# Performance work log

Measured on AMD Instinct MI355X. Metric: run time of the kernel, lower is better.

Reference implementation:

```python
import jax, jax.numpy as jnp
import numpy as np

STATE_DIM = 128
FEATURES = 768
DT_MIN, DT_MAX = 0.001, 0.1


def setup_inputs() -> dict:
    key = jax.random.key(0)
    ks = jax.random.split(key, 8)
    B, S, F, N = 8, 4096, FEATURES, STATE_DIM
    n = jnp.arange(N, dtype=jnp.float32)
    # HiPPO-diag inits (deterministic)
    log_A_real = jnp.log(n + 0.5)
    A_imag = jnp.pi * n
    # lecun_normal: std = 1/sqrt(fan_in), fan_in = axis -2
    B_re = jax.random.normal(ks[0], (N, F), jnp.float32) / jnp.sqrt(N)
    B_im = jax.random.normal(ks[1], (N, F), jnp.float32) / jnp.sqrt(N)
    C_re = jax.random.normal(ks[2], (F, N), jnp.float32) / jnp.sqrt(F)
    C_im = jax.random.normal(ks[3], (F, N), jnp.float32) / jnp.sqrt(F)
    D = jax.random.normal(ks[4], (F,), jnp.float32)
    log_dt = jax.random.uniform(ks[5], (N,), jnp.float32,
                                minval=jnp.log(DT_MIN), maxval=jnp.log(DT_MAX))
    u = jax.random.normal(ks[6], (B, S, F), jnp.float32)
    return {"u": u, "log_A_real": log_A_real, "A_imag": A_imag,
            "B_re": B_re, "B_im": B_im, "C_re": C_re, "C_im": C_im,
            "D": D, "log_dt": log_dt}


def reference(u, log_A_real, A_imag, B_re, B_im, C_re, C_im, D, log_dt):
    B, S, F = u.shape
    N = log_A_real.shape[0]
    dt = jnp.exp(log_dt)                           # [N]
    A_diag = -jnp.exp(log_A_real) + 1j * A_imag    # [N] complex
    A_bar = jnp.exp(A_diag * dt)                   # [N] discretized A
    B_complex = B_re + 1j * B_im                   # [N, F]
    B_bar = (A_bar[:, None] - 1.0) / (A_diag[:, None] + 1e-08) * B_complex
    C_complex = C_re + 1j * C_im                   # [F, N]

    u_f = u.astype(jnp.float32)
    Bu = jnp.einsum('bsf,nf->bsn', u_f, B_bar)     # [B, S, N] complex
    A_exp = jnp.broadcast_to(A_bar[None, None, :], (B, S, N))

    def binary_operator(e1, e2):
        a1, b1 = e1
        a2, b2 = e2
        return (a1 * a2, a2 * b1 + b2)

    _, x_states = jax.lax.associative_scan(binary_operator, (A_exp, Bu), axis=1)
    y = jnp.einsum('fn,bsn->bsf', C_complex, x_states).real
    y = y + D[None, None, :] * u_f
    return y.astype(u.dtype)
```

## Files before the change

kernel.cpp:

```cpp
#include <hip/hip_runtime.h>
#include <hip/hip_bf16.h>
#include <math.h>

typedef __attribute__((ext_vector_type(8))) short short8;
typedef __attribute__((ext_vector_type(4))) float f32x4;
typedef __attribute__((ext_vector_type(4))) unsigned int uint4v;

constexpr int kF = 768;
constexpr int kN = 128;
constexpr int kB = 8;
constexpr int kS = 4096;
constexpr int kM = kB * kS;
constexpr int kChunks = 128;
constexpr int kClen = 32;

constexpr size_t kOffBw      = 3072;
constexpr size_t kOffCw      = 396288;
constexpr size_t kOffFinals  = 789504;
constexpr size_t kOffCarries = 1838080;
constexpr size_t kOffBu      = 2886656;

__device__ __forceinline__ unsigned short f2bf(float f) {
    unsigned int u = __builtin_bit_cast(unsigned int, f);
    u += 0x7fffu + ((u >> 16) & 1u);
    return (unsigned short)(u >> 16);
}
__device__ __forceinline__ float bf2f(unsigned short s) {
    unsigned int u = ((unsigned int)s) << 16;
    return __builtin_bit_cast(float, u);
}

__global__ __launch_bounds__(128)
void pre1(const float* __restrict__ log_A_real, const float* __restrict__ A_imag,
          const float* __restrict__ log_dt, float* __restrict__ ws) {
    int n = threadIdx.x;
    float dt = expf(log_dt[n]);
    float ar = -expf(log_A_real[n]);
    float ai = A_imag[n];
    float er = expf(ar * dt);
    float Ar = er * cosf(ai * dt);
    float Ai = er * sinf(ai * dt);
    float dr = ar + 1e-8f, di = ai;
    float inv = 1.0f / (dr * dr + di * di);
    float nr = Ar - 1.0f, ni = Ai;
    float cr = (nr * dr + ni * di) * inv;
    float ci = (ni * dr - nr * di) * inv;
    float pr = 1.f, pi = 0.f;
    for (int i = 0; i < kClen; ++i) {
        float t = pr * Ar - pi * Ai;
        pi = pr * Ai + pi * Ar;
        pr = t;
    }
    ws[n] = Ar;        ws[128 + n] = Ai;
    ws[256 + n] = pr;  ws[384 + n] = pi;
    ws[512 + n] = cr;  ws[640 + n] = ci;
}

__global__ __launch_bounds__(256)
void pre2(const float* __restrict__ B_re, const float* __restrict__ B_im,
          const float* __restrict__ wsf, unsigned short* __restrict__ bw) {
    int id = blockIdx.x * 256 + threadIdx.x;
    int c = id / kF;
    int f = id - c * kF;
    int n = c & 127;
    float cr = wsf[512 + n], ci = wsf[640 + n];
    float br = B_re[n * kF + f], bi = B_im[n * kF + f];
    float v = (c < 128) ? (cr * br - ci * bi) : (cr * bi + ci * br);
    bw[id] = f2bf(v);
}

__global__ __launch_bounds__(256)
void pre3(const float* __restrict__ C_re, const float* __restrict__ C_im,
          unsigned short* __restrict__ cw) {
    int id = blockIdx.x * 256 + threadIdx.x;
    int f = id >> 8;
    int k = id & 255;
    float v = (k < 128) ? C_re[f * kN + k] : -C_im[f * kN + (k - 128)];
    cw[id] = f2bf(v);
}

template<bool EPI>
__global__ __launch_bounds__(256, 3)
void mfma_gemm(const float* __restrict__ A,
               const unsigned short* __restrict__ W,
               float* __restrict__ Cout, int M, int Nc, int K,
               const float* __restrict__ Dp, const float* __restrict__ Up) {
    __shared__ __align__(16) short As[2][128 * 40];
    __shared__ __align__(16) short Bs[2][128 * 40];

    const int gx = gridDim.x;
    const int nwg = gx * gridDim.y;
    const int orig = blockIdx.y * gx + blockIdx.x;
    const int cpx = nwg >> 3;
    const int sw = (orig & 7) * cpx + (orig >> 3);
    const int m0 = (sw / gx) * 128;
    const int n0 = (sw % gx) * 128;

    const int t = threadIdx.x;
    const int sr = t >> 1;
    const int sh = t & 1;

    const int wave = t >> 6, lane = t & 63;
    const int wr = wave >> 1, wc = wave & 1;
    const int lr = lane & 15, lg = lane >> 4;

    f32x4 acc[4][4] = {};
    const int KT = K >> 5;

    f32x4 avf[4];
    uint4v wv0, wv1;

    auto load_tile = [&](int kt) {
        const int k0 = kt << 5;
        const float* ap = A + (size_t)(m0 + sr) * K + k0 + sh * 16;
        avf[0] = *(const f32x4*)(ap);
        avf[1] = *(const f32x4*)(ap + 4);
        avf[2] = *(const f32x4*)(ap + 8);
        avf[3] = *(const f32x4*)(ap + 12);
        const unsigned short* wp = W + (size_t)(n0 + sr) * K + k0 + sh * 16;
        wv0 = *(const uint4v*)(wp);
        wv1 = *(const uint4v*)(wp + 8);
    };

    auto write_tile = [&](int buf) {
        short h[16];
#pragma unroll
        for (int v = 0; v < 4; ++v)
#pragma unroll
            for (int e = 0; e < 4; ++e)
                h[v * 4 + e] = (short)f2bf(avf[v][e]);
        const int o = sr * 40 + sh * 16;
        *(short8*)(&As[buf][o])     = *(short8*)(&h[0]);
        *(short8*)(&As[buf][o + 8]) = *(short8*)(&h[8]);
        *(short8*)(&Bs[buf][o])     = *(short8*)(&wv0);
        *(short8*)(&Bs[buf][o + 8]) = *(short8*)(&wv1);
    };

    load_tile(0);
    for (int kt = 0; kt < KT; ++kt) {
        const int buf = kt & 1;
        write_tile(buf);
        if (kt + 1 < KT) load_tile(kt + 1);
        __syncthreads();
        short8 ah[4], bh[4];
#pragma unroll
        for (int i = 0; i < 4; ++i) {
            ah[i] = *(const short8*)(&As[buf][(wr * 64 + i * 16 + lr) * 40 + lg * 8]);
            bh[i] = *(const short8*)(&Bs[buf][(wc * 64 + i * 16 + lr) * 40 + lg * 8]);
        }
#pragma unroll
        for (int i = 0; i < 4; ++i)
#pragma unroll
            for (int j = 0; j < 4; ++j)
                acc[i][j] = __builtin_amdgcn_mfma_f32_16x16x32_bf16(ah[i], bh[j], acc[i][j], 0, 0, 0);
    }

#pragma unroll
    for (int i = 0; i < 4; ++i)
#pragma unroll
        for (int j = 0; j < 4; ++j) {
            const int col = n0 + wc * 64 + j * 16 + lr;
#pragma unroll
            for (int q = 0; q < 4; ++q) {
                const int row = m0 + wr * 64 + i * 16 + lg * 4 + q;
                float v = acc[i][j][q];
                if (EPI) v = fmaf(Dp[col], Up[(size_t)row * Nc + col], v);
                Cout[(size_t)row * Nc + col] = v;
            }
        }
}

__global__ __launch_bounds__(128)
void scanA(const float* __restrict__ Bu, const float* __restrict__ wsc,
           float* __restrict__ finals) {
    int n = threadIdx.x;
    int blk = blockIdx.x;
    int b = blk >> 7, c = blk & 127;
    float Ar = wsc[n], Ai = wsc[128 + n];
    float xr = 0.f, xi = 0.f;
    size_t base = ((size_t)(b * kS + c * kClen)) * 256;
    for (int s = 0; s < kClen; ++s) {
        float br = Bu[base + n], bi = Bu[base + 128 + n];
        float tr = Ar * xr - Ai * xi + br;
        xi = Ar * xi + Ai * xr + bi;
        xr = tr;
        base += 256;
    }
    finals[(size_t)blk * 256 + n] = xr;
    finals[(size_t)blk * 256 + 128 + n] = xi;
}

__global__ __launch_bounds__(128)
void scanB(const float* __restrict__ finals, const float* __restrict__ ws,
           float* __restrict__ carries) {
    int n = threadIdx.x;
    int b = blockIdx.x;
    float Pr = ws[256 + n], Pi = ws[384 + n];
    float xr = 0.f, xi = 0.f;
    for (int c = 0; c < kChunks; ++c) {
        size_t o = ((size_t)(b * kChunks + c)) * 256;
        carries[o + n] = xr;
        carries[o + 128 + n] = xi;
        float fr = finals[o + n], fi = finals[o + 128 + n];
        float tr = Pr * xr - Pi * xi + fr;
        xi = Pr * xi + Pi * xr + fi;
        xr = tr;
    }
}

__global__ __launch_bounds__(128)
void scanC(float* __restrict__ Bu, const float* __restrict__ wsc,
           const float* __restrict__ carries) {
    int n = threadIdx.x;
    int blk = blockIdx.x;
    int b = blk >> 7, c = blk & 127;
    float Ar = wsc[n], Ai = wsc[128 + n];
    size_t co = (size_t)blk * 256;
    float xr = carries[co + n], xi = carries[co + 128 + n];
    size_t base = ((size_t)(b * kS + c * kClen)) * 256;
    for (int s = 0; s < kClen; ++s) {
        float br = Bu[base + n], bi = Bu[base + 128 + n];
        float tr = Ar * xr - Ai * xi + br;
        xi = Ar * xi + Ai * xr + bi;
        xr = tr;
        Bu[base + n] = xr;
        Bu[base + 128 + n] = xi;
        base += 256;
    }
}

extern "C" void kernel_launch(void* const* d_in, const int* in_sizes, int n_in,
                              void* d_out, int out_size, void* d_ws, size_t ws_size,
                              hipStream_t stream) {
    const float* u          = (const float*)d_in[0];
    const float* log_A_real = (const float*)d_in[1];
    const float* A_imag     = (const float*)d_in[2];
    const float* B_re       = (const float*)d_in[3];
    const float* B_im       = (const float*)d_in[4];
    const float* C_re       = (const float*)d_in[5];
    const float* C_im       = (const float*)d_in[6];
    const float* D          = (const float*)d_in[7];
    const float* log_dt     = (const float*)d_in[8];

    char* wsb = (char*)d_ws;
    float* wsf            = (float*)wsb;
    unsigned short* bw    = (unsigned short*)(wsb + kOffBw);
    unsigned short* cw    = (unsigned short*)(wsb + kOffCw);
    float* finals         = (float*)(wsb + kOffFinals);
    float* carries        = (float*)(wsb + kOffCarries);
    float* Bu             = (float*)(wsb + kOffBu);
    float* y              = (float*)d_out;

    pre1<<<1, 128, 0, stream>>>(log_A_real, A_imag, log_dt, wsf);
    pre2<<<(256 * kF) / 256, 256, 0, stream>>>(B_re, B_im, wsf, bw);
    pre3<<<(kF * 256) / 256, 256, 0, stream>>>(C_re, C_im, cw);

    mfma_gemm<false><<<dim3(2, kM / 128), 256, 0, stream>>>(
        u, bw, Bu, kM, 256, kF, nullptr, nullptr);

    scanA<<<kB * kChunks, 128, 0, stream>>>(Bu, wsf, finals);
    scanB<<<kB, 128, 0, stream>>>(finals, wsf, carries);
    scanC<<<kB * kChunks, 128, 0, stream>>>(Bu, wsf, carries);

    mfma_gemm<true><<<dim3(kF / 128, kM / 128), 256, 0, stream>>>(
        Bu, cw, y, kM, kF, 256, D, u);
}
```

Before: 110.1 us.

## Fuse input projection GEMM with chunked scan using decoupled lookback

Merges the Bu GEMM and the three scan kernels into a single kernel. Each 512-thread block computes a full 128x256 tile of Bu, scans it in shared memory in four 32-step sub-chunks, and publishes its chunk final with a release flag. It then spins on earlier chunks' flags to gather a carry using a precomputed A^128 power. This removes the Bu round trips through global memory and three launches. The cost is 138KB of shared memory per block, serial waits between chunks that depend on blocks being scheduled in order, a memset for the flags, and a double-buffered K loop with explicit waitcnt barriers in both GEMMs.

```diff
diff --git a/kernel.cpp b/kernel.cpp
--- a/kernel.cpp
+++ b/kernel.cpp
@@ -11,24 +11,24 @@
 constexpr int kB = 8;
 constexpr int kS = 4096;
 constexpr int kM = kB * kS;
-constexpr int kChunks = 128;
-constexpr int kClen = 32;
-
-constexpr size_t kOffBw      = 3072;
-constexpr size_t kOffCw      = 396288;
-constexpr size_t kOffFinals  = 789504;
-constexpr size_t kOffCarries = 1838080;
-constexpr size_t kOffBu      = 2886656;
+
+constexpr size_t kOffBw     = 4096;
+constexpr size_t kOffCw     = 397312;
+constexpr size_t kOffFinals = 790528;
+constexpr size_t kOffFlags  = 1052672;
+constexpr size_t kOffX      = 1053696;
 
 __device__ __forceinline__ unsigned short f2bf(float f) {
     unsigned int u = __builtin_bit_cast(unsigned int, f);
     u += 0x7fffu + ((u >> 16) & 1u);
     return (unsigned short)(u >> 16);
 }
-__device__ __forceinline__ float bf2f(unsigned short s) {
-    unsigned int u = ((unsigned int)s) << 16;
-    return __builtin_bit_cast(float, u);
-}
+
+#define LGKM0_BAR() do { \
+    asm volatile("s_waitcnt lgkmcnt(0)" ::: "memory"); \
+    __builtin_amdgcn_s_barrier(); \
+    __builtin_amdgcn_sched_barrier(0); \
+} while (0)
 
 __global__ __launch_bounds__(128)
 void pre1(const float* __restrict__ log_A_real, const float* __restrict__ A_imag,
@@ -46,14 +46,17 @@
     float cr = (nr * dr + ni * di) * inv;
     float ci = (ni * dr - nr * di) * inv;
     float pr = 1.f, pi = 0.f;
-    for (int i = 0; i < kClen; ++i) {
+    for (int i = 0; i < 32; ++i) {
         float t = pr * Ar - pi * Ai;
         pi = pr * Ai + pi * Ar;
         pr = t;
     }
+    float sr = pr * pr - pi * pi, si = 2.f * pr * pi;
+    float qr = sr * sr - si * si, qi = 2.f * sr * si;
     ws[n] = Ar;        ws[128 + n] = Ai;
     ws[256 + n] = pr;  ws[384 + n] = pi;
     ws[512 + n] = cr;  ws[640 + n] = ci;
+    ws[768 + n] = qr;  ws[896 + n] = qi;
 }
 
 __global__ __launch_bounds__(256)
@@ -79,14 +82,205 @@
     cw[id] = f2bf(v);
 }
 
-template<bool EPI>
+__global__ __launch_bounds__(512, 2)
+void gemm1_scan(const float* __restrict__ A,
+                const unsigned short* __restrict__ W,
+                float* __restrict__ xout,
+                float* __restrict__ finals,
+                unsigned int* __restrict__ flags,
+                const float* __restrict__ wsf) {
+    constexpr int K  = kF;
+    constexpr int KT = K / 32;
+    __shared__ __align__(16) char smem[141312];
+    short* As0 = (short*)smem;
+    short* As1 = As0 + 128 * 40;
+    short* Ws0 = As1 + 128 * 40;
+    short* Ws1 = Ws0 + 256 * 40;
+    float* xbuf = (float*)smem;
+    float* gbuf = (float*)(smem + 133120);
+    float* sbuf = (float*)(smem + 137216);
+
+    const int blk = blockIdx.x;
+    const int m0  = blk * 128;
+    const int b   = blk >> 5;
+    const int ci  = blk & 31;
+
+    const int t = threadIdx.x;
+    const int arow = t >> 2, aq = t & 3;
+    const int wrow = t >> 1, wh = t & 1;
+
+    const int wave = t >> 6, lane = t & 63;
+    const int wm = wave >> 2, wn = wave & 3;
+    const int lr = lane & 15, lg = lane >> 4;
+
+    f32x4 acc[4][4] = {};
+
+    f32x4 aA0, aA1, aB0, aB1;
+    uint4v wA0, wA1, wB0, wB1;
+    const float* aptr = A + (size_t)(m0 + arow) * K + aq * 8;
+    const unsigned short* wptr = W + (size_t)wrow * K + wh * 16;
+
+#define G1_LOAD(SET, kt) do { \
+    const float* p_ = aptr + (kt) * 32; \
+    a##SET##0 = *(const f32x4*)p_; a##SET##1 = *(const f32x4*)(p_ + 4); \
+    const unsigned short* q_ = wptr + (kt) * 32; \
+    w##SET##0 = *(const uint4v*)q_; w##SET##1 = *(const uint4v*)(q_ + 8); \
+} while (0)
+
+#define G1_WRITE(Asb, Wsb, a0, a1, w0, w1) do { \
+    short h_[8]; \
+    _Pragma("unroll") for (int e_ = 0; e_ < 4; ++e_) { \
+        h_[e_]     = (short)f2bf(a0[e_]); \
+        h_[4 + e_] = (short)f2bf(a1[e_]); \
+    } \
+    *(short8*)(&Asb[arow * 40 + aq * 8]) = *(short8*)h_; \
+    *(short8*)(&Wsb[wrow * 40 + wh * 16])     = *(short8*)&w0; \
+    *(short8*)(&Wsb[wrow * 40 + wh * 16 + 8]) = *(short8*)&w1; \
+} while (0)
+
+#define G1_MMA(Asb, Wsb) do { \
+    short8 ah_[4], bh_[4]; \
+    _Pragma("unroll") for (int i_ = 0; i_ < 4; ++i_) { \
+        ah_[i_] = *(const short8*)(&Asb[(wm * 64 + i_ * 16 + lr) * 40 + lg * 8]); \
+        bh_[i_] = *(const short8*)(&Wsb[(wn * 64 + i_ * 16 + lr) * 40 + lg * 8]); \
+    } \
+    _Pragma("unroll") for (int i_ = 0; i_ < 4; ++i_) \
+    _Pragma("unroll") for (int j_ = 0; j_ < 4; ++j_) \
+        acc[i_][j_] = __builtin_amdgcn_mfma_f32_16x16x32_bf16(ah_[i_], bh_[j_], acc[i_][j_], 0, 0, 0); \
+} while (0)
+
+    G1_LOAD(A, 0);
+    G1_LOAD(B, 1);
+    for (int kt = 0; kt < KT; kt += 2) {
+        G1_WRITE(As0, Ws0, aA0, aA1, wA0, wA1);
+        if (kt + 2 < KT) G1_LOAD(A, kt + 2);
+        LGKM0_BAR();
+        G1_MMA(As0, Ws0);
+        G1_WRITE(As1, Ws1, aB0, aB1, wB0, wB1);
+        if (kt + 3 < KT) G1_LOAD(B, kt + 3);
+        LGKM0_BAR();
+        G1_MMA(As1, Ws1);
+    }
+
+    __syncthreads();
+#pragma unroll
+    for (int i = 0; i < 4; ++i)
+#pragma unroll
+        for (int j = 0; j < 4; ++j) {
+            const int col = wn * 64 + j * 16 + lr;
+#pragma unroll
+            for (int q = 0; q < 4; ++q)
+                xbuf[(wm * 64 + i * 16 + lg * 4 + q) * 260 + col] = acc[i][j][q];
+        }
+    __syncthreads();
+
+    const int sq = t >> 7;
+    const int sn = t & 127;
+    const float Ar = wsf[sn], Ai = wsf[128 + sn];
+    {
+        float xr = 0.f, xi = 0.f;
+        const int r0 = sq * 32;
+        for (int tt = 0; tt < 32; ++tt) {
+            float* pr = &xbuf[(r0 + tt) * 260 + sn];
+            float* pim = &xbuf[(r0 + tt) * 260 + 128 + sn];
+            float br = *pr, bi = *pim;
+            float trr = Ar * xr - Ai * xi + br;
+            xi = Ar * xi + Ai * xr + bi;
+            xr = trr;
+            *pr = xr; *pim = xi;
+        }
+        gbuf[(sq * 2 + 0) * 128 + sn] = xr;
+        gbuf[(sq * 2 + 1) * 128 + sn] = xi;
+    }
+    __syncthreads();
+
+    if (t < 128) {
+        const float P1r = wsf[256 + sn], P1i = wsf[384 + sn];
+        float fr = 0.f, fi = 0.f;
+#pragma unroll
+        for (int q = 0; q < 4; ++q) {
+            float gr = gbuf[(q * 2 + 0) * 128 + sn];
+            float gi = gbuf[(q * 2 + 1) * 128 + sn];
+            float trr = P1r * fr - P1i * fi + gr;
+            fi = P1r * fi + P1i * fr + gi;
+            fr = trr;
+        }
+        finals[(size_t)blk * 256 + sn]       = fr;
+        finals[(size_t)blk * 256 + 128 + sn] = fi;
+        __threadfence();
+    }
+    __syncthreads();
+    if (t == 0)
+        __hip_atomic_store(&flags[blk], 1u, __ATOMIC_RELEASE, __HIP_MEMORY_SCOPE_AGENT);
+
+    if (t < ci) {
+        const unsigned int* fp = &flags[b * 32 + t];
+        while (__hip_atomic_load(fp, __ATOMIC_ACQUIRE, __HIP_MEMORY_SCOPE_AGENT) == 0u)
+            __builtin_amdgcn_s_sleep(1);
+        __threadfence();
+    }
+    __syncthreads();
+
+    if (t < 128) {
+        const float P4r = wsf[768 + sn], P4i = wsf[896 + sn];
+        float cr = 0.f, cii = 0.f;
+        for (int j = 0; j < ci; ++j) {
+            size_t o = (size_t)(b * 32 + j) * 256;
+            float fr = finals[o + sn], fi = finals[o + 128 + sn];
+            float trr = P4r * cr - P4i * cii + fr;
+            cii = P4r * cii + P4i * cr + fi;
+            cr = trr;
+        }
+        const float P1r = wsf[256 + sn], P1i = wsf[384 + sn];
+        float sr = cr, si = cii;
+#pragma unroll
+        for (int q = 0; q < 4; ++q) {
+            sbuf[(q * 2 + 0) * 128 + sn] = sr;
+            sbuf[(q * 2 + 1) * 128 + sn] = si;
+            float gr = gbuf[(q * 2 + 0) * 128 + sn];
+            float gi = gbuf[(q * 2 + 1) * 128 + sn];
+            float trr = P1r * sr - P1i * si + gr;
+            si = P1r * si + P1i * sr + gi;
+            sr = trr;
+        }
+    }
+    __syncthreads();
+
+    {
+        float sr = sbuf[(sq * 2 + 0) * 128 + sn];
+        float si = sbuf[(sq * 2 + 1) * 128 + sn];
+        float cr = sr, cii = si;
+        const int r0 = sq * 32;
+        for (int tt = 0; tt < 32; ++tt) {
+            float trr = Ar * cr - Ai * cii;
+            cii = Ar * cii + Ai * cr;
+            cr = trr;
+            xbuf[(r0 + tt) * 260 + sn]       += cr;
+            xbuf[(r0 + tt) * 260 + 128 + sn] += cii;
+        }
+    }
+    __syncthreads();
+
+    {
+        const int orow = t >> 2, opart = t & 3;
+        float* dst = xout + (size_t)(m0 + orow) * 256 + opart * 64;
+        const float* src = &xbuf[orow * 260 + opart * 64];
+#pragma unroll
+        for (int v = 0; v < 16; ++v)
+            *(f32x4*)(dst + v * 4) = *(const f32x4*)(src + v * 4);
+    }
+}
+
 __global__ __launch_bounds__(256, 3)
-void mfma_gemm(const float* __restrict__ A,
-               const unsigned short* __restrict__ W,
-               float* __restrict__ Cout, int M, int Nc, int K,
-               const float* __restrict__ Dp, const float* __restrict__ Up) {
-    __shared__ __align__(16) short As[2][128 * 40];
-    __shared__ __align__(16) short Bs[2][128 * 40];
+void gemm2(const float* __restrict__ A,
+           const unsigned short* __restrict__ W,
+           float* __restrict__ Cout,
+           const float* __restrict__ Dp, const float* __restrict__ Up) {
+    constexpr int K = 256, KT = 8, Nc = kF;
+    __shared__ __align__(16) short As0[128 * 40];
+    __shared__ __align__(16) short As1[128 * 40];
+    __shared__ __align__(16) short Ws0[128 * 40];
+    __shared__ __align__(16) short Ws1[128 * 40];
 
     const int gx = gridDim.x;
     const int nwg = gx * gridDim.y;
@@ -97,62 +291,64 @@
     const int n0 = (sw % gx) * 128;
 
     const int t = threadIdx.x;
-    const int sr = t >> 1;
-    const int sh = t & 1;
+    const int sr = t >> 1, sh = t & 1;
 
     const int wave = t >> 6, lane = t & 63;
     const int wr = wave >> 1, wc = wave & 1;
     const int lr = lane & 15, lg = lane >> 4;
 
     f32x4 acc[4][4] = {};
-    const int KT = K >> 5;
-
-    f32x4 avf[4];
-    uint4v wv0, wv1;
-
-    auto load_tile = [&](int kt) {
-        const int k0 = kt << 5;
-        const float* ap = A + (size_t)(m0 + sr) * K + k0 + sh * 16;
-        avf[0] = *(const f32x4*)(ap);
-        avf[1] = *(const f32x4*)(ap + 4);
-        avf[2] = *(const f32x4*)(ap + 8);
-        avf[3] = *(const f32x4*)(ap + 12);
-        const unsigned short* wp = W + (size_t)(n0 + sr) * K + k0 + sh * 16;
-        wv0 = *(const uint4v*)(wp);
-        wv1 = *(const uint4v*)(wp + 8);
-    };
-
-    auto write_tile = [&](int buf) {
-        short h[16];
-#pragma unroll
-        for (int v = 0; v < 4; ++v)
-#pragma unroll
-            for (int e = 0; e < 4; ++e)
-                h[v * 4 + e] = (short)f2bf(avf[v][e]);
-        const int o = sr * 40 + sh * 16;
-        *(short8*)(&As[buf][o])     = *(short8*)(&h[0]);
-        *(short8*)(&As[buf][o + 8]) = *(short8*)(&h[8]);
-        *(short8*)(&Bs[buf][o])     = *(short8*)(&wv0);
-        *(short8*)(&Bs[buf][o + 8]) = *(short8*)(&wv1);
-    };
-
-    load_tile(0);
-    for (int kt = 0; kt < KT; ++kt) {
-        const int buf = kt & 1;
-        write_tile(buf);
-        if (kt + 1 < KT) load_tile(kt + 1);
-        __syncthreads();
-        short8 ah[4], bh[4];
-#pragma unroll
-        for (int i = 0; i < 4; ++i) {
-            ah[i] = *(const short8*)(&As[buf][(wr * 64 + i * 16 + lr) * 40 + lg * 8]);
-            bh[i] = *(const short8*)(&Bs[buf][(wc * 64 + i * 16 + lr) * 40 + lg * 8]);
-        }
-#pragma unroll
-        for (int i = 0; i < 4; ++i)
-#pragma unroll
-            for (int j = 0; j < 4; ++j)
-                acc[i][j] = __builtin_amdgcn_mfma_f32_16x16x32_bf16(ah[i], bh[j], acc[i][j], 0, 0, 0);
+
+    f32x4 aA0, aA1, aA2, aA3, aB0, aB1, aB2, aB3;
+    uint4v wA0, wA1, wB0, wB1;
+    const float* aptr = A + (size_t)(m0 + sr) * K + sh * 16;
+    const unsigned short* wptr = W + (size_t)(n0 + sr) * K + sh * 16;
+
+#define G2_LOAD(SET, kt) do { \
+    const float* p_ = aptr + (kt) * 32; \
+    a##SET##0 = *(const f32x4*)p_;        a##SET##1 = *(const f32x4*)(p_ + 4); \
+    a##SET##2 = *(const f32x4*)(p_ + 8);  a##SET##3 = *(const f32x4*)(p_ + 12); \
+    const unsigned short* q_ = wptr + (kt) * 32; \
+    w##SET##0 = *(const uint4v*)q_; w##SET##1 = *(const uint4v*)(q_ + 8); \
+} while (0)
+
+#define G2_WRITE(Asb, Wsb, a0, a1, a2, a3, w0, w1) do { \
+    short h_[16]; \
+    _Pragma("unroll") for (int e_ = 0; e_ < 4; ++e_) { \
+        h_[e_]      = (short)f2bf(a0[e_]); \
+        h_[4 + e_]  = (short)f2bf(a1[e_]); \
+        h_[8 + e_]  = (short)f2bf(a2[e_]); \
+        h_[12 + e_] = (short)f2bf(a3[e_]); \
+    } \
+    const int o_ = sr * 40 + sh * 16; \
+    *(short8*)(&Asb[o_])     = *(short8*)&h_[0]; \
+    *(short8*)(&Asb[o_ + 8]) = *(short8*)&h_[8]; \
+    *(short8*)(&Wsb[o_])     = *(short8*)&w0; \
+    *(short8*)(&Wsb[o_ + 8]) = *(short8*)&w1; \
+} while (0)
+
+#define G2_MMA(Asb, Wsb) do { \
+    short8 ah_[4], bh_[4]; \
+    _Pragma("unroll") for (int i_ = 0; i_ < 4; ++i_) { \
+        ah_[i_] = *(const short8*)(&Asb[(wr * 64 + i_ * 16 + lr) * 40 + lg * 8]); \
+        bh_[i_] = *(const short8*)(&Wsb[(wc * 64 + i_ * 16 + lr) * 40 + lg * 8]); \
+    } \
+    _Pragma("unroll") for (int i_ = 0; i_ < 4; ++i_) \
+    _Pragma("unroll") for (int j_ = 0; j_ < 4; ++j_) \
+        acc[i_][j_] = __builtin_amdgcn_mfma_f32_16x16x32_bf16(ah_[i_], bh_[j_], acc[i_][j_], 0, 0, 0); \
+} while (0)
+
+    G2_LOAD(A, 0);
+    G2_LOAD(B, 1);
+    for (int kt = 0; kt < KT; kt += 2) {
+        G2_WRITE(As0, Ws0, aA0, aA1, aA2, aA3, wA0, wA1);
+        if (kt + 2 < KT) G2_LOAD(A, kt + 2);
+        LGKM0_BAR();
+        G2_MMA(As0, Ws0);
+        G2_WRITE(As1, Ws1, aB0, aB1, aB2, aB3, wB0, wB1);
+        if (kt + 3 < KT) G2_LOAD(B, kt + 3);
+        LGKM0_BAR();
+        G2_MMA(As1, Ws1);
     }
 
 #pragma unroll
@@ -164,69 +360,10 @@
             for (int q = 0; q < 4; ++q) {
                 const int row = m0 + wr * 64 + i * 16 + lg * 4 + q;
                 float v = acc[i][j][q];
-                if (EPI) v = fmaf(Dp[col], Up[(size_t)row * Nc + col], v);
+                v = fmaf(Dp[col], Up[(size_t)row * Nc + col], v);
                 Cout[(size_t)row * Nc + col] = v;
             }
         }
-}
-
-__global__ __launch_bounds__(128)
-void scanA(const float* __restrict__ Bu, const float* __restrict__ wsc,
-           float* __restrict__ finals) {
-    int n = threadIdx.x;
-    int blk = blockIdx.x;
-    int b = blk >> 7, c = blk & 127;
-    float Ar = wsc[n], Ai = wsc[128 + n];
-    float xr = 0.f, xi = 0.f;
-    size_t base = ((size_t)(b * kS + c * kClen)) * 256;
-    for (int s = 0; s < kClen; ++s) {
-        float br = Bu[base + n], bi = Bu[base + 128 + n];
-        float tr = Ar * xr - Ai * xi + br;
-        xi = Ar * xi + Ai * xr + bi;
-        xr = tr;
-        base += 256;
-    }
-    finals[(size_t)blk * 256 + n] = xr;
-    finals[(size_t)blk * 256 + 128 + n] = xi;
-}
-
-__global__ __launch_bounds__(128)
-void scanB(const float* __restrict__ finals, const float* __restrict__ ws,
-           float* __restrict__ carries) {
-    int n = threadIdx.x;
-    int b = blockIdx.x;
-    float Pr = ws[256 + n], Pi = ws[384 + n];
-    float xr = 0.f, xi = 0.f;
-    for (int c = 0; c < kChunks; ++c) {
-        size_t o = ((size_t)(b * kChunks + c)) * 256;
-        carries[o + n] = xr;
-        carries[o + 128 + n] = xi;
-        float fr = finals[o + n], fi = finals[o + 128 + n];
-        float tr = Pr * xr - Pi * xi + fr;
-        xi = Pr * xi + Pi * xr + fi;
-        xr = tr;
-    }
-}
-
-__global__ __launch_bounds__(128)
-void scanC(float* __restrict__ Bu, const float* __restrict__ wsc,
-           const float* __restrict__ carries) {
-    int n = threadIdx.x;
-    int blk = blockIdx.x;
-    int b = blk >> 7, c = blk & 127;
-    float Ar = wsc[n], Ai = wsc[128 + n];
-    size_t co = (size_t)blk * 256;
-    float xr = carries[co + n], xi = carries[co + 128 + n];
-    size_t base = ((size_t)(b * kS + c * kClen)) * 256;
-    for (int s = 0; s < kClen; ++s) {
-        float br = Bu[base + n], bi = Bu[base + 128 + n];
-        float tr = Ar * xr - Ai * xi + br;
-        xi = Ar * xi + Ai * xr + bi;
-        xr = tr;
-        Bu[base + n] = xr;
-        Bu[base + 128 + n] = xi;
-        base += 256;
-    }
 }
 
 extern "C" void kernel_launch(void* const* d_in, const int* in_sizes, int n_in,
@@ -247,21 +384,17 @@
     unsigned short* bw    = (unsigned short*)(wsb + kOffBw);
     unsigned short* cw    = (unsigned short*)(wsb + kOffCw);
     float* finals         = (float*)(wsb + kOffFinals);
-    float* carries        = (float*)(wsb + kOffCarries);
-    float* Bu             = (float*)(wsb + kOffBu);
+    unsigned int* flags   = (unsigned int*)(wsb + kOffFlags);
+    float* x              = (float*)(wsb + kOffX);
     float* y              = (float*)d_out;
+
+    hipMemsetAsync(flags, 0, 256 * sizeof(unsigned int), stream);
 
     pre1<<<1, 128, 0, stream>>>(log_A_real, A_imag, log_dt, wsf);
     pre2<<<(256 * kF) / 256, 256, 0, stream>>>(B_re, B_im, wsf, bw);
     pre3<<<(kF * 256) / 256, 256, 0, stream>>>(C_re, C_im, cw);
 
-    mfma_gemm<false><<<dim3(2, kM / 128), 256, 0, stream>>>(
-        u, bw, Bu, kM, 256, kF, nullptr, nullptr);
-
-    scanA<<<kB * kChunks, 128, 0, stream>>>(Bu, wsf, finals);
-    scanB<<<kB, 128, 0, stream>>>(finals, wsf, carries);
-    scanC<<<kB * kChunks, 128, 0, stream>>>(Bu, wsf, carries);
-
-    mfma_gemm<true><<<dim3(kF / 128, kM / 128), 256, 0, stream>>>(
-        Bu, cw, y, kM, kF, 256, D, u);
-}
+    gemm1_scan<<<kM / 128, 512, 0, stream>>>(u, bw, x, finals, flags, wsf);
+
+    gemm2<<<dim3(kF / 128, kM / 128), 256, 0, stream>>>(x, cw, y, D, u);
+}
```

After: 129.3 us. 1.17x slower.

## Store scanned states as bf16 and specialize both GEMMs with explicit double-buffering

Applied to the files above, without the earlier changes.

scanC now writes the scanned complex states as bf16 into a separate buffer instead of overwriting fp32 Bu. The second GEMM reads this bf16 directly, so it skips the fp32 load and convert step and moves half as many bytes. Bu is now staged in the output buffer, which shrinks workspace use. Both GEMMs are split into dedicated kernels with constant K, two named register load sets and explicit LDS-wait barriers, and the scan loops get unroll pragmas. The extra bf16 rounding on the states before the C projection slightly increases numerical error.

```diff
diff --git a/kernel.cpp b/kernel.cpp
--- a/kernel.cpp
+++ b/kernel.cpp
@@ -14,21 +14,23 @@
 constexpr int kChunks = 128;
 constexpr int kClen = 32;
 
-constexpr size_t kOffBw      = 3072;
-constexpr size_t kOffCw      = 396288;
-constexpr size_t kOffFinals  = 789504;
-constexpr size_t kOffCarries = 1838080;
-constexpr size_t kOffBu      = 2886656;
+constexpr size_t kOffBw      = 4096;
+constexpr size_t kOffCw      = 397312;
+constexpr size_t kOffFinals  = 790528;
+constexpr size_t kOffCarries = 1052672;
+constexpr size_t kOffXbf     = 1314816;
 
 __device__ __forceinline__ unsigned short f2bf(float f) {
     unsigned int u = __builtin_bit_cast(unsigned int, f);
     u += 0x7fffu + ((u >> 16) & 1u);
     return (unsigned short)(u >> 16);
 }
-__device__ __forceinline__ float bf2f(unsigned short s) {
-    unsigned int u = ((unsigned int)s) << 16;
-    return __builtin_bit_cast(float, u);
-}
+
+#define LGKM0_BAR() do { \
+    asm volatile("s_waitcnt lgkmcnt(0)" ::: "memory"); \
+    __builtin_amdgcn_s_barrier(); \
+    __builtin_amdgcn_sched_barrier(0); \
+} while (0)
 
 __global__ __launch_bounds__(128)
 void pre1(const float* __restrict__ log_A_real, const float* __restrict__ A_imag,
@@ -79,14 +81,15 @@
     cw[id] = f2bf(v);
 }
 
-template<bool EPI>
-__global__ __launch_bounds__(256, 3)
-void mfma_gemm(const float* __restrict__ A,
-               const unsigned short* __restrict__ W,
-               float* __restrict__ Cout, int M, int Nc, int K,
-               const float* __restrict__ Dp, const float* __restrict__ Up) {
-    __shared__ __align__(16) short As[2][128 * 40];
-    __shared__ __align__(16) short Bs[2][128 * 40];
+__global__ __launch_bounds__(256, 2)
+void gemm1(const float* __restrict__ A,
+           const unsigned short* __restrict__ W,
+           float* __restrict__ Cout) {
+    constexpr int K = kF, KT = K / 32;
+    __shared__ __align__(16) short As0[128 * 40];
+    __shared__ __align__(16) short As1[128 * 40];
+    __shared__ __align__(16) short Ws0[128 * 40];
+    __shared__ __align__(16) short Ws1[128 * 40];
 
     const int gx = gridDim.x;
     const int nwg = gx * gridDim.y;
@@ -97,62 +100,64 @@
     const int n0 = (sw % gx) * 128;
 
     const int t = threadIdx.x;
-    const int sr = t >> 1;
-    const int sh = t & 1;
+    const int sr = t >> 1, sh = t & 1;
 
     const int wave = t >> 6, lane = t & 63;
     const int wr = wave >> 1, wc = wave & 1;
     const int lr = lane & 15, lg = lane >> 4;
 
     f32x4 acc[4][4] = {};
-    const int KT = K >> 5;
-
-    f32x4 avf[4];
-    uint4v wv0, wv1;
-
-    auto load_tile = [&](int kt) {
-        const int k0 = kt << 5;
-        const float* ap = A + (size_t)(m0 + sr) * K + k0 + sh * 16;
-        avf[0] = *(const f32x4*)(ap);
-        avf[1] = *(const f32x4*)(ap + 4);
-        avf[2] = *(const f32x4*)(ap + 8);
-        avf[3] = *(const f32x4*)(ap + 12);
-        const unsigned short* wp = W + (size_t)(n0 + sr) * K + k0 + sh * 16;
-        wv0 = *(const uint4v*)(wp);
-        wv1 = *(const uint4v*)(wp + 8);
-    };
-
-    auto write_tile = [&](int buf) {
-        short h[16];
-#pragma unroll
-        for (int v = 0; v < 4; ++v)
-#pragma unroll
-            for (int e = 0; e < 4; ++e)
-                h[v * 4 + e] = (short)f2bf(avf[v][e]);
-        const int o = sr * 40 + sh * 16;
-        *(short8*)(&As[buf][o])     = *(short8*)(&h[0]);
-        *(short8*)(&As[buf][o + 8]) = *(short8*)(&h[8]);
-        *(short8*)(&Bs[buf][o])     = *(short8*)(&wv0);
-        *(short8*)(&Bs[buf][o + 8]) = *(short8*)(&wv1);
-    };
-
-    load_tile(0);
-    for (int kt = 0; kt < KT; ++kt) {
-        const int buf = kt & 1;
-        write_tile(buf);
-        if (kt + 1 < KT) load_tile(kt + 1);
-        __syncthreads();
-        short8 ah[4], bh[4];
-#pragma unroll
-        for (int i = 0; i < 4; ++i) {
-            ah[i] = *(const short8*)(&As[buf][(wr * 64 + i * 16 + lr) * 40 + lg * 8]);
-            bh[i] = *(const short8*)(&Bs[buf][(wc * 64 + i * 16 + lr) * 40 + lg * 8]);
-        }
-#pragma unroll
-        for (int i = 0; i < 4; ++i)
-#pragma unroll
-            for (int j = 0; j < 4; ++j)
-                acc[i][j] = __builtin_amdgcn_mfma_f32_16x16x32_bf16(ah[i], bh[j], acc[i][j], 0, 0, 0);
+
+    f32x4 aA0, aA1, aA2, aA3, aB0, aB1, aB2, aB3;
+    uint4v wA0, wA1, wB0, wB1;
+    const float* aptr = A + (size_t)(m0 + sr) * K + sh * 16;
+    const unsigned short* wptr = W + (size_t)(n0 + sr) * K + sh * 16;
+
+#define G1_LOAD(SET, kt) do { \
+    const float* p_ = aptr + (kt) * 32; \
+    a##SET##0 = *(const f32x4*)p_;        a##SET##1 = *(const f32x4*)(p_ + 4); \
+    a##SET##2 = *(const f32x4*)(p_ + 8);  a##SET##3 = *(const f32x4*)(p_ + 12); \
+    const unsigned short* q_ = wptr + (kt) * 32; \
+    w##SET##0 = *(const uint4v*)q_; w##SET##1 = *(const uint4v*)(q_ + 8); \
+} while (0)
+
+#define G1_WRITE(Asb, Wsb, a0, a1, a2, a3, w0, w1) do { \
+    short h_[16]; \
+    _Pragma("unroll") for (int e_ = 0; e_ < 4; ++e_) { \
+        h_[e_]      = (short)f2bf(a0[e_]); \
+        h_[4 + e_]  = (short)f2bf(a1[e_]); \
+        h_[8 + e_]  = (short)f2bf(a2[e_]); \
+        h_[12 + e_] = (short)f2bf(a3[e_]); \
+    } \
+    const int o_ = sr * 40 + sh * 16; \
+    *(short8*)(&Asb[o_])     = *(short8*)&h_[0]; \
+    *(short8*)(&Asb[o_ + 8]) = *(short8*)&h_[8]; \
+    *(short8*)(&Wsb[o_])     = *(short8*)&w0; \
+    *(short8*)(&Wsb[o_ + 8]) = *(short8*)&w1; \
+} while (0)
+
+#define G1_MMA(Asb, Wsb) do { \
+    short8 ah_[4], bh_[4]; \
+    _Pragma("unroll") for (int i_ = 0; i_ < 4; ++i_) { \
+        ah_[i_] = *(const short8*)(&Asb[(wr * 64 + i_ * 16 + lr) * 40 + lg * 8]); \
+        bh_[i_] = *(const short8*)(&Wsb[(wc * 64 + i_ * 16 + lr) * 40 + lg * 8]); \
+    } \
+    _Pragma("unroll") for (int i_ = 0; i_ < 4; ++i_) \
+    _Pragma("unroll") for (int j_ = 0; j_ < 4; ++j_) \
+        acc[i_][j_] = __builtin_amdgcn_mfma_f32_16x16x32_bf16(ah_[i_], bh_[j_], acc[i_][j_], 0, 0, 0); \
+} while (0)
+
+    G1_LOAD(A, 0);
+    G1_LOAD(B, 1);
+    for (int kt = 0; kt < KT; kt += 2) {
+        G1_WRITE(As0, Ws0, aA0, aA1, aA2, aA3, wA0, wA1);
+        if (kt + 2 < KT) G1_LOAD(A, kt + 2);
+        LGKM0_BAR();
+        G1_MMA(As0, Ws0);
+        G1_WRITE(As1, Ws1, aB0, aB1, aB2, aB3, wB0, wB1);
+        if (kt + 3 < KT) G1_LOAD(B, kt + 3);
+        LGKM0_BAR();
+        G1_MMA(As1, Ws1);
     }
 
 #pragma unroll
@@ -163,11 +168,12 @@
 #pragma unroll
             for (int q = 0; q < 4; ++q) {
                 const int row = m0 + wr * 64 + i * 16 + lg * 4 + q;
-                float v = acc[i][j][q];
-                if (EPI) v = fmaf(Dp[col], Up[(size_t)row * Nc + col], v);
-                Cout[(size_t)row * Nc + col] = v;
+                Cout[(size_t)row * 256 + col] = acc[i][j][q];
             }
         }
+#undef G1_LOAD
+#undef G1_WRITE
+#undef G1_MMA
 }
 
 __global__ __launch_bounds__(128)
@@ -179,6 +185,7 @@
     float Ar = wsc[n], Ai = wsc[128 + n];
     float xr = 0.f, xi = 0.f;
     size_t base = ((size_t)(b * kS + c * kClen)) * 256;
+#pragma unroll 8
     for (int s = 0; s < kClen; ++s) {
         float br = Bu[base + n], bi = Bu[base + 128 + n];
         float tr = Ar * xr - Ai * xi + br;
@@ -197,6 +204,7 @@
     int b = blockIdx.x;
     float Pr = ws[256 + n], Pi = ws[384 + n];
     float xr = 0.f, xi = 0.f;
+#pragma unroll 8
     for (int c = 0; c < kChunks; ++c) {
         size_t o = ((size_t)(b * kChunks + c)) * 256;
         carries[o + n] = xr;
@@ -209,8 +217,8 @@
 }
 
 __global__ __launch_bounds__(128)
-void scanC(float* __restrict__ Bu, const float* __restrict__ wsc,
-           const float* __restrict__ carries) {
+void scanC(const float* __restrict__ Bu, const float* __restrict__ wsc,
+           const float* __restrict__ carries, unsigned short* __restrict__ xbf) {
     int n = threadIdx.x;
     int blk = blockIdx.x;
     int b = blk >> 7, c = blk & 127;
@@ -218,15 +226,106 @@
     size_t co = (size_t)blk * 256;
     float xr = carries[co + n], xi = carries[co + 128 + n];
     size_t base = ((size_t)(b * kS + c * kClen)) * 256;
+#pragma unroll 4
     for (int s = 0; s < kClen; ++s) {
         float br = Bu[base + n], bi = Bu[base + 128 + n];
         float tr = Ar * xr - Ai * xi + br;
         xi = Ar * xi + Ai * xr + bi;
         xr = tr;
-        Bu[base + n] = xr;
-        Bu[base + 128 + n] = xi;
+        xbf[base + n]       = f2bf(xr);
+        xbf[base + 128 + n] = f2bf(xi);
         base += 256;
     }
+}
+
+__global__ __launch_bounds__(256, 3)
+void gemm2(const unsigned short* __restrict__ A,
+           const unsigned short* __restrict__ W,
+           float* __restrict__ Cout,
+           const float* __restrict__ Dp, const float* __restrict__ Up) {
+    constexpr int K = 256, KT = 8, Nc = kF;
+    __shared__ __align__(16) short As0[128 * 40];
+    __shared__ __align__(16) short As1[128 * 40];
+    __shared__ __align__(16) short Ws0[128 * 40];
+    __shared__ __align__(16) short Ws1[128 * 40];
+
+    const int gx = gridDim.x;
+    const int nwg = gx * gridDim.y;
+    const int orig = blockIdx.y * gx + blockIdx.x;
+    const int cpx = nwg >> 3;
+    const int sw = (orig & 7) * cpx + (orig >> 3);
+    const int m0 = (sw / gx) * 128;
+    const int n0 = (sw % gx) * 128;
+
+    const int t = threadIdx.x;
+    const int sr = t >> 1, sh = t & 1;
+
+    const int wave = t >> 6, lane = t & 63;
+    const int wr = wave >> 1, wc = wave & 1;
+    const int lr = lane & 15, lg = lane >> 4;
+
+    f32x4 acc[4][4] = {};
+
+    uint4v aA0, aA1, aB0, aB1;
+    uint4v wA0, wA1, wB0, wB1;
+    const unsigned short* aptr = A + (size_t)(m0 + sr) * K + sh * 16;
+    const unsigned short* wptr = W + (size_t)(n0 + sr) * K + sh * 16;
+
+#define G2_LOAD(SET, kt) do { \
+    const unsigned short* p_ = aptr + (kt) * 32; \
+    a##SET##0 = *(const uint4v*)p_; a##SET##1 = *(const uint4v*)(p_ + 8); \
+    const unsigned short* q_ = wptr + (kt) * 32; \
+    w##SET##0 = *(const uint4v*)q_; w##SET##1 = *(const uint4v*)(q_ + 8); \
+} while (0)
+
+#define G2_WRITE(Asb, Wsb, a0, a1, w0, w1) do { \
+    const int o_ = sr * 40 + sh * 16; \
+    *(short8*)(&Asb[o_])     = *(short8*)&a0; \
+    *(short8*)(&Asb[o_ + 8]) = *(short8*)&a1; \
+    *(short8*)(&Wsb[o_])     = *(short8*)&w0; \
+    *(short8*)(&Wsb[o_ + 8]) = *(short8*)&w1; \
+} while (0)
+
+#define G2_MMA(Asb, Wsb) do { \
+    short8 ah_[4], bh_[4]; \
+    _Pragma("unroll") for (int i_ = 0; i_ < 4; ++i_) { \
+        ah_[i_] = *(const short8*)(&Asb[(wr * 64 + i_ * 16 + lr) * 40 + lg * 8]); \
+        bh_[i_] = *(const short8*)(&Wsb[(wc * 64 + i_ * 16 + lr) * 40 + lg * 8]); \
+    } \
+    _Pragma("unroll") for (int i_ = 0; i_ < 4; ++i_) \
+    _Pragma("unroll") for (int j_ = 0; j_ < 4; ++j_) \
+        acc[i_][j_] = __builtin_amdgcn_mfma_f32_16x16x32_bf16(ah_[i_], bh_[j_], acc[i_][j_], 0, 0, 0); \
+} while (0)
+
+    G2_LOAD(A, 0);
+    G2_LOAD(B, 1);
+    for (int kt = 0; kt < KT; kt += 2) {
+        G2_WRITE(As0, Ws0, aA0, aA1, wA0, wA1);
+        if (kt + 2 < KT) G2_LOAD(A, kt + 2);
+        LGKM0_BAR();
+        G2_MMA(As0, Ws0);
+        G2_WRITE(As1, Ws1, aB0, aB1, wB0, wB1);
+        if (kt + 3 < KT) G2_LOAD(B, kt + 3);
+        LGKM0_BAR();
+        G2_MMA(As1, Ws1);
+    }
+
+#pragma unroll
+    for (int i = 0; i < 4; ++i)
+#pragma unroll
+        for (int j = 0; j < 4; ++j) {
+            const int col = n0 + wc * 64 + j * 16 + lr;
+#pragma unroll
+            for (int q = 0; q < 4; ++q) {
+                const int row = m0 + wr * 64 + i * 16 + lg * 4 + q;
+                float v = acc[i][j][q];
+                v = fmaf(Dp[col], Up[(size_t)row * Nc + col], v);
+                Cout[(size_t)row * Nc + col] = v;
+            }
+        }
+#undef G2_LOAD
+#undef G2_WRITE
+#undef G2_MMA
 }
 
 extern "C" void kernel_launch(void* const* d_in, const int* in_sizes, int n_in,
@@ -248,20 +347,19 @@
     unsigned short* cw    = (unsigned short*)(wsb + kOffCw);
     float* finals         = (float*)(wsb + kOffFinals);
     float* carries        = (float*)(wsb + kOffCarries);
-    float* Bu             = (float*)(wsb + kOffBu);
+    unsigned short* xbf   = (unsigned short*)(wsb + kOffXbf);
     float* y              = (float*)d_out;
+    float* Bu             = (float*)d_out;
 
     pre1<<<1, 128, 0, stream>>>(log_A_real, A_imag, log_dt, wsf);
     pre2<<<(256 * kF) / 256, 256, 0, stream>>>(B_re, B_im, wsf, bw);
     pre3<<<(kF * 256) / 256, 256, 0, stream>>>(C_re, C_im, cw);
 
-    mfma_gemm<false><<<dim3(2, kM / 128), 256, 0, stream>>>(
-        u, bw, Bu, kM, 256, kF, nullptr, nullptr);
+    gemm1<<<dim3(2, kM / 128), 256, 0, stream>>>(u, bw, Bu);
 
     scanA<<<kB * kChunks, 128, 0, stream>>>(Bu, wsf, finals);
     scanB<<<kB, 128, 0, stream>>>(finals, wsf, carries);
-    scanC<<<kB * kChunks, 128, 0, stream>>>(Bu, wsf, carries);
-
-    mfma_gemm<true><<<dim3(kF / 128, kM / 128), 256, 0, stream>>>(
-        Bu, cw, y, kM, kF, 256, D, u);
-}
+    scanC<<<kB * kChunks, 128, 0, stream>>>(Bu, wsf, carries, xbf);
+
+    gemm2<<<dim3(kF / 128, kM / 128), 256, 0, stream>>>(xbf, cw, y, D, u);
+}
```

Measured after the change: 102.2 us. 1.08x faster.
